# Optimization experiments

Hardware: AMD Instinct MI355X
Metric: run time of the kernel (lower is better)

The kernel has to match this reference:

```python
import jax, jax.numpy as jnp
import numpy as np

N, H, HD = 512, 8, 128          # n_nodes, n_heads, h feature dim
M0, M1 = 256, 256               # mlp_units
NORM_CONST = 1.0


def setup_inputs() -> dict:
    key = jax.random.key(0)
    ks = jax.random.split(key, 16)
    def w(k, i, o, scale=1.0):
        return jax.random.normal(k, (i, o), jnp.float32) * (scale / np.sqrt(i))
    F = HD + H * H               # h_concat dim = 128 + 64 = 192
    EIN = H + 2 * F              # edge MLP input dim = 8 + 384 = 392
    return {
        "x": jax.random.normal(ks[0], (N, H, 3), jnp.float32),
        "h": jax.random.normal(ks[1], (N, HD), jnp.float32),
        # phi_e: MLP([256,256], silu, activate_final=True)
        "We0": w(ks[2], EIN, M0), "be0": jnp.zeros((M0,), jnp.float32),
        "We1": w(ks[3], M0, M1), "be1": jnp.zeros((M1,), jnp.float32),
        # phi_inf: Linear(1) + sigmoid
        "Winf": w(ks[4], M1, 1), "binf": jnp.zeros((1,), jnp.float32),
        # phi_x: MLP([256,256], silu, activate_final=True) -> Linear(n_heads) (variance-scaled small init)
        "Wx0": w(ks[5], M1, M0), "bx0": jnp.zeros((M0,), jnp.float32),
        "Wx1": w(ks[6], M0, M1), "bx1": jnp.zeros((M1,), jnp.float32),
        "Wxo": w(ks[7], M1, H, scale=0.03), "bxo": jnp.zeros((H,), jnp.float32),
        # phi_h: MLP([256,256], silu, activate_final=False)... note haiku MLP applies
        # activation between layers; final Linear(h_dim) appended in forward.
        "Wh0": w(ks[8], M1 + HD, M0), "bh0": jnp.zeros((M0,), jnp.float32),
        "Wh1": w(ks[9], M0, M1), "bh1": jnp.zeros((M1,), jnp.float32),
        "Who": w(ks[10], M1, HD), "bho": jnp.zeros((HD,), jnp.float32),
    }


def _forward(x, h, We0, be0, We1, be1, Winf, binf, Wx0, bx0, Wx1, bx1,
             Wxo, bxo, Wh0, bh0, Wh1, bh1, Who, bho):
    n, nh = x.shape[0], x.shape[1]
    silu = jax.nn.silu
    off = 1.0 - jnp.eye(n, dtype=x.dtype)                  # off-diagonal node mask
    # per-node head-pair squared distances -> [N, H*H] (diag naturally 0)
    dh = x[:, :, None, :] - x[:, None, :, :]               # [N,H,H,3]
    sqh = jnp.sum(dh * dh, axis=-1).reshape(n, nh * nh)
    hc = jnp.concatenate([h, sqh], axis=-1)                # [N, F]
    # all-pairs node diffs per head: dn[i,j,h] = x[j,h] - x[i,h]
    dn = x[None] - x[:, None]                              # [N,N,H,3]
    sqn = jnp.sum(dn * dn, axis=-1)                        # [N,N,H]
    F = hc.shape[-1]
    hc_j = jnp.broadcast_to(hc[None], (n, n, F))           # receiver-side: hc[j]
    hc_i = jnp.broadcast_to(hc[:, None], (n, n, F))        # sender-side: hc[i]
    edge_in = jnp.concatenate([sqn, hc_j, hc_i], axis=-1)  # [N,N,H+2F]
    # phi_e (activate_final=True), zero self-edges
    m = silu(silu(edge_in @ We0 + be0) @ We1 + be1) * off[:, :, None]
    # gate + message aggregation
    e = jax.nn.sigmoid(m @ Winf + binf)[..., 0] * off      # [N,N]
    m_i = jnp.einsum('ijd,ij->id', m, e)                   # [N,M1]
    # phi_x multi-head coordinate weights (tanh=False), zero self-edges
    px = (silu(silu(m @ Wx0 + bx0) @ Wx1 + bx1) @ Wxo + bxo) * off[:, :, None]
    # normalize_by_x_norm=True path
    norm = jnp.sqrt(sqn + 1e-8) + NORM_CONST               # [N,N,H]
    ndiff = (dn / norm[..., None]) * off[:, :, None, None]
    shift = jnp.einsum('ijhd,ijh->ihd', ndiff, px) / (n - 1)  # agg='mean'
    x_new = x + shift
    # phi_h with residual
    ph_in = jnp.concatenate([m_i, h], axis=-1)
    h_new = h + silu(silu(ph_in @ Wh0 + bh0) @ Wh1 + bh1) @ Who + bho
    return x_new, h_new


def reference(x, h, We0, be0, We1, be1, Winf, binf, Wx0, bx0, Wx1, bx1,
              Wxo, bxo, Wh0, bh0, Wh1, bh1, Who, bho):
    return _forward(x, h, We0, be0, We1, be1, Winf, binf, Wx0, bx0, Wx1, bx1,
                    Wxo, bxo, Wh0, bh0, Wh1, bh1, Who, bho)
```

## Files before the change

kernel.cpp:

```cpp
#include <hip/hip_runtime.h>
#include <math.h>

#define N_NODES 512
#define NH 8
#define HD 128
#define M 256
#define PITCH 264
#define JTILE 64
#define RPW 16

typedef __bf16 v8bf __attribute__((ext_vector_type(8)));
typedef float f32x4 __attribute__((ext_vector_type(4)));
typedef unsigned short us4v __attribute__((ext_vector_type(4)));

__device__ __forceinline__ float silu_f(float v) {
  return v * __builtin_amdgcn_rcpf(1.f + __expf(-v));
}
__device__ __forceinline__ float sigmoid_f(float v) {
  return __builtin_amdgcn_rcpf(1.f + __expf(-v));
}
__device__ __forceinline__ unsigned short f2bf(float f) {
  unsigned u = __float_as_uint(f);
  u += 0x7fffu + ((u >> 16) & 1u);
  return (unsigned short)(u >> 16);
}
__device__ __forceinline__ unsigned short f2bf_hi(float f) {
  return (unsigned short)((__float_as_uint(f) + 0x8000u) >> 16);
}
__device__ __forceinline__ float bf2f(unsigned short s) {
  return __uint_as_float(((unsigned)s) << 16);
}

__device__ __forceinline__ void gl2lds16(const unsigned short* g, unsigned short* l) {
  __builtin_amdgcn_global_load_lds(
      (const __attribute__((address_space(1))) unsigned int*)g,
      (__attribute__((address_space(3))) unsigned int*)l, 16, 0, 0);
}

__global__ __launch_bounds__(256) void k_pre(
    const float* __restrict__ x, const float* __restrict__ h,
    const float* __restrict__ We0, const float* __restrict__ be0,
    const float* __restrict__ We1, const float* __restrict__ Wx0,
    const float* __restrict__ Wx1, const float* __restrict__ Wxo,
    unsigned short* __restrict__ wsB,
    float* __restrict__ P, float* __restrict__ Q,
    float* __restrict__ mi, float* __restrict__ shift)
{
  const int t = threadIdx.x;
  if (blockIdx.x < 816) {
    const int gid = blockIdx.x * 256 + t;
    if (gid >= 208896) return;
    float val;
    int dst;
    if (gid < 196608) {
      const int layer = gid >> 16, e = gid & 65535;
      const int k = e >> 8, n = e & 255;
      const float* W = (layer == 0) ? We1 : (layer == 1) ? Wx0 : Wx1;
      val = W[e];
      const int kt = k >> 5, w = k & 31, quad = w >> 3, j = w & 7;
      const int nt = n >> 4, lnib = n & 15;
      dst = layer * 65536 + ((kt * 16 + nt) * 64 + quad * 16 + lnib) * 8 + j;
    } else if (gid < 198656) {
      const int e = gid - 196608;
      val = Wxo[e];
      const int k = e >> 3, col = e & 7;
      const int kt = k >> 5, w = k & 31, quad = w >> 3, j = w & 7;
      dst = 196608 + (kt * 64 + quad * 16 + col) * 8 + j;
    } else if (gid < 200704) {
      const int e = gid - 198656;
      val = 0.f;
      const int k = e >> 3, col = e & 7;
      const int kt = k >> 5, w = k & 31, quad = w >> 3, j = w & 7;
      dst = 196608 + (kt * 64 + quad * 16 + col + 8) * 8 + j;
    } else if (gid < 202752) {
      const int e = gid - 200704;
      val = We0[e];
      const int j = e >> 8, n = e & 255, nt = n >> 4, lnib = n & 15;
      dst = 200704 + (nt * 64 + lnib) * 8 + j;
    } else {
      const int e = gid - 202752;
      val = 0.f;
      const int q = 1 + (e >> 11), rem = e & 2047;
      const int j = rem & 7, lnib = (rem >> 3) & 15, nt = rem >> 7;
      dst = 200704 + (nt * 64 + q * 16 + lnib) * 8 + j;
    }
    wsB[dst] = f2bf(val);
    return;
  }
  const int i = blockIdx.x - 816;
  __shared__ float s_x[24];
  __shared__ float s_hc[192];
  mi[i * M + t] = 0.f;
  if (t < 24) { shift[i * 24 + t] = 0.f; s_x[t] = x[i * 24 + t]; }
  __syncthreads();
  if (t < HD) {
    s_hc[t] = h[i * HD + t];
  } else if (t < 192) {
    const int p = t - HD, a = p >> 3, b = p & 7;
    float s = 0.f;
#pragma unroll
    for (int d = 0; d < 3; ++d) {
      const float dx = s_x[a * 3 + d] - s_x[b * 3 + d];
      s = fmaf(dx, dx, s);
    }
    s_hc[t] = s;
  }
  __syncthreads();
  float p = 0.f, q = 0.f;
  for (int k = 0; k < 192; ++k) {
    const float hv = s_hc[k];
    p = fmaf(hv, We0[(8 + k) * M + t], p);
    q = fmaf(hv, We0[(200 + k) * M + t], q);
  }
  P[i * M + t] = p;
  Q[i * M + t] = q + be0[t];
}

__global__ __launch_bounds__(512, 4) void k_edge(
    const float* __restrict__ x,
    const float* __restrict__ P, const float* __restrict__ Q,
    const float* __restrict__ be1,
    const float* __restrict__ Winf, const float* __restrict__ binf,
    const float* __restrict__ bx0, const float* __restrict__ bx1,
    const float* __restrict__ bxo,
    const unsigned short* __restrict__ wsB,
    float* __restrict__ mi_acc, float* __restrict__ shift_acc)
{
  const int i  = blockIdx.x;
  const int j0 = blockIdx.y * JTILE;
  const int t  = threadIdx.x;
  const int lane = t & 63, wave = t >> 6;
  const int lnib = lane & 15, quad = lane >> 4;
  const int rg = wave >> 1, c = wave & 1;
  const int r0 = rg * RPW;
  const int jw = j0 + r0;
  const int cb = c * 128;

  __shared__ __align__(16) unsigned short a_act[JTILE * PITCH];
  __shared__ __align__(16) unsigned short B_buf[2][8192];
  __shared__ __align__(16) float s_sqn[JTILE][8];
  __shared__ __align__(16) unsigned short s_sqnb[JTILE][8];
  __shared__ float s_red[JTILE][2];
  __shared__ float s_e[JTILE];

  auto stage = [&](const unsigned short* __restrict__ Bg, int kt, int which) {
    const unsigned short* src = Bg + kt * 8192 + wave * 1024 + lane * 8;
    unsigned short* dst = &B_buf[which][wave * 1024];
    gl2lds16(src,       dst);
    gl2lds16(src + 512, dst + 512);
  };

#pragma unroll
  for (int kk = 0; kk < 2; ++kk) {
    const int idx = kk * 64 + lane;
    const int r = idx >> 3, hh = idx & 7;
    const int j = jw + r;
    float s = 0.f;
#pragma unroll
    for (int d = 0; d < 3; ++d) {
      const float dx = x[j * 24 + hh * 3 + d] - x[i * 24 + hh * 3 + d];
      s = fmaf(dx, dx, s);
    }
    s_sqn[r0 + r][hh] = s;
    s_sqnb[r0 + r][hh] = f2bf(s);
  }

  stage(wsB, 0, 0);

  const float binf0 = binf[0];

  f32x4 acc[8];

  {
#pragma unroll
    for (int nt = 0; nt < 8; ++nt)
#pragma unroll
      for (int reg = 0; reg < 4; ++reg)
        acc[nt][reg] = P[(jw + quad * 4 + reg) * M + cb + nt * 16 + lnib];
    const v8bf aS = *(const v8bf*)&s_sqnb[r0 + lnib][0];
    const unsigned short* B0 = wsB + 200704;
#pragma unroll
    for (int nt = 0; nt < 8; ++nt) {
      const v8bf bv = *(const v8bf*)&B0[((c * 8 + nt) * 64 + lane) * 8];
      acc[nt] = __builtin_amdgcn_mfma_f32_16x16x32_bf16(aS, bv, acc[nt], 0, 0, 0);
    }
#pragma unroll
    for (int nt = 0; nt < 8; ++nt) {
      const float qv = Q[i * M + cb + nt * 16 + lnib];
#pragma unroll
      for (int reg = 0; reg < 4; ++reg) {
        const int row = r0 + quad * 4 + reg;
        a_act[row * PITCH + cb + nt * 16 + lnib] = f2bf_hi(silu_f(acc[nt][reg] + qv));
      }
    }
  }

  auto run_gemm = [&](const unsigned short* __restrict__ Bg,
                      const unsigned short* __restrict__ Bnext) {
    __syncthreads();
#pragma unroll
    for (int kt = 0; kt < 8; ++kt) {
      if (kt < 7)      stage(Bg, kt + 1, (kt + 1) & 1);
      else if (Bnext)  stage(Bnext, 0, 0);
      const v8bf a0 = *(const v8bf*)&a_act[(r0 + lnib) * PITCH + kt * 32 + quad * 8];
#pragma unroll
      for (int nt = 0; nt < 8; ++nt) {
        const v8bf bv = *(const v8bf*)&B_buf[kt & 1][(c * 8 + nt) * 512 + lane * 8];
        acc[nt] = __builtin_amdgcn_mfma_f32_16x16x32_bf16(a0, bv, acc[nt], 0, 0, 0);
      }
      __syncthreads();
    }
  };

#pragma unroll
  for (int nt = 0; nt < 8; ++nt) {
    const float b = be1[cb + nt * 16 + lnib];
    acc[nt] = (f32x4){b, b, b, b};
  }
  run_gemm(wsB, wsB + 65536);
  {
    float ge[4] = {0.f, 0.f, 0.f, 0.f};
#pragma unroll
    for (int nt = 0; nt < 8; ++nt) {
      const float wfv = Winf[cb + nt * 16 + lnib];
#pragma unroll
      for (int reg = 0; reg < 4; ++reg) {
        float v = silu_f(acc[nt][reg]);
        const int row = r0 + quad * 4 + reg;
        if (j0 + row == i) v = 0.f;
        a_act[row * PITCH + cb + nt * 16 + lnib] = f2bf_hi(v);
        ge[reg] = fmaf(v, wfv, ge[reg]);
      }
    }
#pragma unroll
    for (int reg = 0; reg < 4; ++reg) {
      float g = ge[reg];
      g += __shfl_xor(g, 1);
      g += __shfl_xor(g, 2);
      g += __shfl_xor(g, 4);
      g += __shfl_xor(g, 8);
      if (lnib == 0) s_red[r0 + quad * 4 + reg][c] = g;
    }
  }
  __syncthreads();
  if (t < JTILE) s_e[t] = sigmoid_f(s_red[t][0] + s_red[t][1] + binf0);
  __syncthreads();

  {
    const int ch = cb + lane * 2;
    float m0 = 0.f, m1 = 0.f;
#pragma unroll
    for (int r = 0; r < RPW; ++r) {
      const unsigned mv = *(const unsigned*)&a_act[(r0 + r) * PITCH + ch];
      const float ev = s_e[r0 + r];
      m0 = fmaf(bf2f((unsigned short)(mv & 0xffffu)), ev, m0);
      m1 = fmaf(bf2f((unsigned short)(mv >> 16)), ev, m1);
    }
    atomicAdd(&mi_acc[i * M + ch + 0], m0);
    atomicAdd(&mi_acc[i * M + ch + 1], m1);
  }

#pragma unroll
  for (int nt = 0; nt < 8; ++nt) {
    const float b = bx0[cb + nt * 16 + lnib];
    acc[nt] = (f32x4){b, b, b, b};
  }
  run_gemm(wsB + 65536, wsB + 131072);
#pragma unroll
  for (int nt = 0; nt < 8; ++nt)
#pragma unroll
    for (int reg = 0; reg < 4; ++reg) {
      const int row = r0 + quad * 4 + reg;
      a_act[row * PITCH + cb + nt * 16 + lnib] = f2bf_hi(silu_f(acc[nt][reg]));
    }

#pragma unroll
  for (int nt = 0; nt < 8; ++nt) {
    const float b = bx1[cb + nt * 16 + lnib];
    acc[nt] = (f32x4){b, b, b, b};
  }
  run_gemm(wsB + 131072, nullptr);
#pragma unroll
  for (int nt = 0; nt < 8; ++nt)
#pragma unroll
    for (int reg = 0; reg < 4; ++reg) {
      const int row = r0 + quad * 4 + reg;
      a_act[row * PITCH + cb + nt * 16 + lnib] = f2bf_hi(silu_f(acc[nt][reg]));
    }
  __syncthreads();

  if (c == 0) {
    f32x4 px;
    {
      const float b = (lnib < 8) ? bxo[lnib] : 0.f;
      px = (f32x4){b, b, b, b};
      const unsigned short* B = wsB + 196608;
#pragma unroll
      for (int kt = 0; kt < 8; ++kt) {
        const v8bf a0 = *(const v8bf*)&a_act[(r0 + lnib) * PITCH + kt * 32 + quad * 8];
        const v8bf bv = *(const v8bf*)&B[(kt * 64 + lane) * 8];
        px = __builtin_amdgcn_mfma_f32_16x16x32_bf16(a0, bv, px, 0, 0, 0);
      }
    }
    const int hh = lnib & 7;
    const float xi0 = x[i * 24 + hh * 3 + 0];
    const float xi1 = x[i * 24 + hh * 3 + 1];
    const float xi2 = x[i * 24 + hh * 3 + 2];
    float p0 = 0.f, p1 = 0.f, p2 = 0.f;
#pragma unroll
    for (int reg = 0; reg < 4; ++reg) {
      const int row = r0 + quad * 4 + reg;
      const int jg = j0 + row;
      if (jg != i) {
        const float pxv = px[reg];
        const float sq  = s_sqn[row][hh];
        const float f   = pxv * __builtin_amdgcn_rcpf(sqrtf(sq + 1e-8f) + 1.f);
        p0 = fmaf(x[jg * 24 + hh * 3 + 0] - xi0, f, p0);
        p1 = fmaf(x[jg * 24 + hh * 3 + 1] - xi1, f, p1);
        p2 = fmaf(x[jg * 24 + hh * 3 + 2] - xi2, f, p2);
      }
    }
    p0 += __shfl_xor(p0, 16); p0 += __shfl_xor(p0, 32);
    p1 += __shfl_xor(p1, 16); p1 += __shfl_xor(p1, 32);
    p2 += __shfl_xor(p2, 16); p2 += __shfl_xor(p2, 32);
    if (lane < 8) {
      atomicAdd(&shift_acc[i * 24 + hh * 3 + 0], p0);
      atomicAdd(&shift_acc[i * 24 + hh * 3 + 1], p1);
      atomicAdd(&shift_acc[i * 24 + hh * 3 + 2], p2);
    }
  }
}

__global__ __launch_bounds__(256) void k_hout(
    const float* __restrict__ x, const float* __restrict__ shift,
    const float* __restrict__ h, const float* __restrict__ mi,
    const float* __restrict__ Wh0, const float* __restrict__ bh0,
    const float* __restrict__ Wh1, const float* __restrict__ bh1,
    const float* __restrict__ Who, const float* __restrict__ bho,
    float* __restrict__ out_x, float* __restrict__ out_h)
{
  const int i = blockIdx.x, t = threadIdx.x;
  __shared__ float s_in[M + HD];
  __shared__ float s_b[M];
  if (t < 24) out_x[i * 24 + t] = x[i * 24 + t] + shift[i * 24 + t] * (1.f / 511.f);
  s_in[t] = mi[i * M + t];
  if (t < HD) s_in[M + t] = h[i * HD + t];
  __syncthreads();
  float acc = bh0[t];
  for (int k = 0; k < M + HD; ++k) acc = fmaf(s_in[k], Wh0[k * M + t], acc);
  s_b[t] = silu_f(acc);
  __syncthreads();
  float acc2 = bh1[t];
  for (int k = 0; k < M; ++k) acc2 = fmaf(s_b[k], Wh1[k * M + t], acc2);
  const float a1v = silu_f(acc2);
  __syncthreads();
  s_in[t] = a1v;
  __syncthreads();
  if (t < HD) {
    float o = bho[t];
    for (int k = 0; k < M; ++k) o = fmaf(s_in[k], Who[k * HD + t], o);
    out_h[i * HD + t] = h[i * HD + t] + o;
  }
}

extern "C" void kernel_launch(void* const* d_in, const int* in_sizes, int n_in,
                              void* d_out, int out_size, void* d_ws, size_t ws_size,
                              hipStream_t stream)
{
  const float* x    = (const float*)d_in[0];
  const float* h    = (const float*)d_in[1];
  const float* We0  = (const float*)d_in[2];
  const float* be0  = (const float*)d_in[3];
  const float* We1  = (const float*)d_in[4];
  const float* be1  = (const float*)d_in[5];
  const float* Winf = (const float*)d_in[6];
  const float* binf = (const float*)d_in[7];
  const float* Wx0  = (const float*)d_in[8];
  const float* bx0  = (const float*)d_in[9];
  const float* Wx1  = (const float*)d_in[10];
  const float* bx1  = (const float*)d_in[11];
  const float* Wxo  = (const float*)d_in[12];
  const float* bxo  = (const float*)d_in[13];
  const float* Wh0  = (const float*)d_in[14];
  const float* bh0  = (const float*)d_in[15];
  const float* Wh1  = (const float*)d_in[16];
  const float* bh1  = (const float*)d_in[17];
  const float* Who  = (const float*)d_in[18];
  const float* bho  = (const float*)d_in[19];

  float* out_x = (float*)d_out;
  float* out_h = out_x + N_NODES * NH * 3;

  float* ws    = (float*)d_ws;
  float* mi    = ws;
  float* shift = ws + 131072;
  float* P     = ws + 143360;
  float* Q     = ws + 274432;
  unsigned short* wsB = (unsigned short*)(ws + 405504);

  k_pre<<<816 + N_NODES, 256, 0, stream>>>(
      x, h, We0, be0, We1, Wx0, Wx1, Wxo, wsB, P, Q, mi, shift);
  k_edge<<<dim3(N_NODES, N_NODES / JTILE), 512, 0, stream>>>(
      x, P, Q, be1, Winf, binf, bx0, bx1, bxo, wsB, mi, shift);
  k_hout<<<N_NODES, 256, 0, stream>>>(
      x, shift, h, mi, Wh0, bh0, Wh1, bh1, Who, bho, out_x, out_h);
}
```

Before: 306.5 us.

## Retile edge GEMM waves to 32x64 blocks and single-buffer weight staging

Changes the per-wave tile in the edge kernel from 16 rows x 128 columns to 32 rows x 64 columns (2 row groups x 4 column groups). Each B fragment now feeds two MFMAs, which cuts LDS reads of the weights per MFMA. The double-buffered B staging with prefetch is replaced by a single buffer with two barriers per k-step, which frees LDS but removes the overlap between global-to-LDS copies and compute. The mi and px reductions are adapted to the new layout.

Result: slower. 324.6 us (+5.9%).

```diff
diff --git a/kernel.cpp b/kernel.cpp
--- a/kernel.cpp
+++ b/kernel.cpp
@@ -7,11 +7,9 @@
 #define M 256
 #define PITCH 264
 #define JTILE 64
-#define RPW 16
 
 typedef __bf16 v8bf __attribute__((ext_vector_type(8)));
 typedef float f32x4 __attribute__((ext_vector_type(4)));
-typedef unsigned short us4v __attribute__((ext_vector_type(4)));
 
 __device__ __forceinline__ float silu_f(float v) {
   return v * __builtin_amdgcn_rcpf(1.f + __expf(-v));
@@ -131,27 +129,27 @@
   const int t  = threadIdx.x;
   const int lane = t & 63, wave = t >> 6;
   const int lnib = lane & 15, quad = lane >> 4;
-  const int rg = wave >> 1, c = wave & 1;
-  const int r0 = rg * RPW;
+  const int rg = wave >> 2, cg = wave & 3;
+  const int r0 = rg * 32;
   const int jw = j0 + r0;
-  const int cb = c * 128;
+  const int cb = cg * 64;
 
   __shared__ __align__(16) unsigned short a_act[JTILE * PITCH];
-  __shared__ __align__(16) unsigned short B_buf[2][8192];
+  __shared__ __align__(16) unsigned short B_buf[8192];
   __shared__ __align__(16) float s_sqn[JTILE][8];
   __shared__ __align__(16) unsigned short s_sqnb[JTILE][8];
-  __shared__ float s_red[JTILE][2];
+  __shared__ float s_red[JTILE][4];
   __shared__ float s_e[JTILE];
 
-  auto stage = [&](const unsigned short* __restrict__ Bg, int kt, int which) {
+  auto stage = [&](const unsigned short* __restrict__ Bg, int kt) {
     const unsigned short* src = Bg + kt * 8192 + wave * 1024 + lane * 8;
-    unsigned short* dst = &B_buf[which][wave * 1024];
+    unsigned short* dst = &B_buf[wave * 1024];
     gl2lds16(src,       dst);
     gl2lds16(src + 512, dst + 512);
   };
 
 #pragma unroll
-  for (int kk = 0; kk < 2; ++kk) {
+  for (int kk = 0; kk < 4; ++kk) {
     const int idx = kk * 64 + lane;
     const int r = idx >> 3, hh = idx & 7;
     const int j = jw + r;
@@ -165,141 +163,172 @@
     s_sqnb[r0 + r][hh] = f2bf(s);
   }
 
-  stage(wsB, 0, 0);
-
   const float binf0 = binf[0];
 
-  f32x4 acc[8];
+  f32x4 acc[2][4];
 
   {
 #pragma unroll
-    for (int nt = 0; nt < 8; ++nt)
-#pragma unroll
-      for (int reg = 0; reg < 4; ++reg)
-        acc[nt][reg] = P[(jw + quad * 4 + reg) * M + cb + nt * 16 + lnib];
-    const v8bf aS = *(const v8bf*)&s_sqnb[r0 + lnib][0];
+    for (int rf = 0; rf < 2; ++rf)
+#pragma unroll
+      for (int nt = 0; nt < 4; ++nt)
+#pragma unroll
+        for (int reg = 0; reg < 4; ++reg)
+          acc[rf][nt][reg] =
+              P[(jw + rf * 16 + quad * 4 + reg) * M + cb + nt * 16 + lnib];
+    const v8bf aS0 = *(const v8bf*)&s_sqnb[r0 + lnib][0];
+    const v8bf aS1 = *(const v8bf*)&s_sqnb[r0 + 16 + lnib][0];
     const unsigned short* B0 = wsB + 200704;
 #pragma unroll
-    for (int nt = 0; nt < 8; ++nt) {
-      const v8bf bv = *(const v8bf*)&B0[((c * 8 + nt) * 64 + lane) * 8];
-      acc[nt] = __builtin_amdgcn_mfma_f32_16x16x32_bf16(aS, bv, acc[nt], 0, 0, 0);
-    }
-#pragma unroll
-    for (int nt = 0; nt < 8; ++nt) {
-      const float qv = Q[i * M + cb + nt * 16 + lnib];
+    for (int nt = 0; nt < 4; ++nt) {
+      const v8bf bv = *(const v8bf*)&B0[((cg * 4 + nt) * 64 + lane) * 8];
+      acc[0][nt] = __builtin_amdgcn_mfma_f32_16x16x32_bf16(aS0, bv, acc[0][nt], 0, 0, 0);
+      acc[1][nt] = __builtin_amdgcn_mfma_f32_16x16x32_bf16(aS1, bv, acc[1][nt], 0, 0, 0);
+    }
+#pragma unroll
+    for (int rf = 0; rf < 2; ++rf)
+#pragma unroll
+      for (int nt = 0; nt < 4; ++nt) {
+        const float qv = Q[i * M + cb + nt * 16 + lnib];
+#pragma unroll
+        for (int reg = 0; reg < 4; ++reg) {
+          const int row = r0 + rf * 16 + quad * 4 + reg;
+          a_act[row * PITCH + cb + nt * 16 + lnib] =
+              f2bf_hi(silu_f(acc[rf][nt][reg] + qv));
+        }
+      }
+  }
+
+  auto run_gemm = [&](const unsigned short* __restrict__ Bg) {
+#pragma unroll
+    for (int kt = 0; kt < 8; ++kt) {
+      __syncthreads();
+      stage(Bg, kt);
+      __syncthreads();
+      const v8bf a0 = *(const v8bf*)&a_act[(r0 + lnib) * PITCH + kt * 32 + quad * 8];
+      const v8bf a1 = *(const v8bf*)&a_act[(r0 + 16 + lnib) * PITCH + kt * 32 + quad * 8];
+#pragma unroll
+      for (int nt = 0; nt < 4; ++nt) {
+        const v8bf bv = *(const v8bf*)&B_buf[(cg * 4 + nt) * 512 + lane * 8];
+        acc[0][nt] = __builtin_amdgcn_mfma_f32_16x16x32_bf16(a0, bv, acc[0][nt], 0, 0, 0);
+        acc[1][nt] = __builtin_amdgcn_mfma_f32_16x16x32_bf16(a1, bv, acc[1][nt], 0, 0, 0);
+      }
+    }
+    __syncthreads();
+  };
+
+#pragma unroll
+  for (int rf = 0; rf < 2; ++rf)
+#pragma unroll
+    for (int nt = 0; nt < 4; ++nt) {
+      const float b = be1[cb + nt * 16 + lnib];
+      acc[rf][nt] = (f32x4){b, b, b, b};
+    }
+  run_gemm(wsB);
+  {
+    float ge[2][4] = {{0.f, 0.f, 0.f, 0.f}, {0.f, 0.f, 0.f, 0.f}};
+#pragma unroll
+    for (int rf = 0; rf < 2; ++rf)
+#pragma unroll
+      for (int nt = 0; nt < 4; ++nt) {
+        const float wfv = Winf[cb + nt * 16 + lnib];
+#pragma unroll
+        for (int reg = 0; reg < 4; ++reg) {
+          float v = silu_f(acc[rf][nt][reg]);
+          const int row = r0 + rf * 16 + quad * 4 + reg;
+          if (j0 + row == i) v = 0.f;
+          a_act[row * PITCH + cb + nt * 16 + lnib] = f2bf_hi(v);
+          ge[rf][reg] = fmaf(v, wfv, ge[rf][reg]);
+        }
+      }
+#pragma unroll
+    for (int rf = 0; rf < 2; ++rf)
 #pragma unroll
       for (int reg = 0; reg < 4; ++reg) {
-        const int row = r0 + quad * 4 + reg;
-        a_act[row * PITCH + cb + nt * 16 + lnib] = f2bf_hi(silu_f(acc[nt][reg] + qv));
-      }
-    }
-  }
-
-  auto run_gemm = [&](const unsigned short* __restrict__ Bg,
-                      const unsigned short* __restrict__ Bnext) {
-    __syncthreads();
-#pragma unroll
-    for (int kt = 0; kt < 8; ++kt) {
-      if (kt < 7)      stage(Bg, kt + 1, (kt + 1) & 1);
-      else if (Bnext)  stage(Bnext, 0, 0);
-      const v8bf a0 = *(const v8bf*)&a_act[(r0 + lnib) * PITCH + kt * 32 + quad * 8];
-#pragma unroll
-      for (int nt = 0; nt < 8; ++nt) {
-        const v8bf bv = *(const v8bf*)&B_buf[kt & 1][(c * 8 + nt) * 512 + lane * 8];
-        acc[nt] = __builtin_amdgcn_mfma_f32_16x16x32_bf16(a0, bv, acc[nt], 0, 0, 0);
-      }
-      __syncthreads();
-    }
-  };
-
-#pragma unroll
-  for (int nt = 0; nt < 8; ++nt) {
-    const float b = be1[cb + nt * 16 + lnib];
-    acc[nt] = (f32x4){b, b, b, b};
-  }
-  run_gemm(wsB, wsB + 65536);
+        float g = ge[rf][reg];
+        g += __shfl_xor(g, 1);
+        g += __shfl_xor(g, 2);
+        g += __shfl_xor(g, 4);
+        g += __shfl_xor(g, 8);
+        if (lnib == 0) s_red[r0 + rf * 16 + quad * 4 + reg][cg] = g;
+      }
+  }
+  __syncthreads();
+  if (t < JTILE)
+    s_e[t] = sigmoid_f(s_red[t][0] + s_red[t][1] + s_red[t][2] + s_red[t][3] + binf0);
+  __syncthreads();
+
   {
-    float ge[4] = {0.f, 0.f, 0.f, 0.f};
-#pragma unroll
-    for (int nt = 0; nt < 8; ++nt) {
-      const float wfv = Winf[cb + nt * 16 + lnib];
-#pragma unroll
-      for (int reg = 0; reg < 4; ++reg) {
-        float v = silu_f(acc[nt][reg]);
-        const int row = r0 + quad * 4 + reg;
-        if (j0 + row == i) v = 0.f;
-        a_act[row * PITCH + cb + nt * 16 + lnib] = f2bf_hi(v);
-        ge[reg] = fmaf(v, wfv, ge[reg]);
-      }
-    }
-#pragma unroll
-    for (int reg = 0; reg < 4; ++reg) {
-      float g = ge[reg];
-      g += __shfl_xor(g, 1);
-      g += __shfl_xor(g, 2);
-      g += __shfl_xor(g, 4);
-      g += __shfl_xor(g, 8);
-      if (lnib == 0) s_red[r0 + quad * 4 + reg][c] = g;
-    }
-  }
-  __syncthreads();
-  if (t < JTILE) s_e[t] = sigmoid_f(s_red[t][0] + s_red[t][1] + binf0);
-  __syncthreads();
-
-  {
-    const int ch = cb + lane * 2;
+    const int ch = cb + (lane & 31) * 2;
+    const int rh = (lane >> 5) * 16;
     float m0 = 0.f, m1 = 0.f;
 #pragma unroll
-    for (int r = 0; r < RPW; ++r) {
-      const unsigned mv = *(const unsigned*)&a_act[(r0 + r) * PITCH + ch];
-      const float ev = s_e[r0 + r];
+    for (int r = 0; r < 16; ++r) {
+      const int row = r0 + rh + r;
+      const unsigned mv = *(const unsigned*)&a_act[row * PITCH + ch];
+      const float ev = s_e[row];
       m0 = fmaf(bf2f((unsigned short)(mv & 0xffffu)), ev, m0);
       m1 = fmaf(bf2f((unsigned short)(mv >> 16)), ev, m1);
     }
-    atomicAdd(&mi_acc[i * M + ch + 0], m0);
-    atomicAdd(&mi_acc[i * M + ch + 1], m1);
-  }
-
-#pragma unroll
-  for (int nt = 0; nt < 8; ++nt) {
-    const float b = bx0[cb + nt * 16 + lnib];
-    acc[nt] = (f32x4){b, b, b, b};
-  }
-  run_gemm(wsB + 65536, wsB + 131072);
-#pragma unroll
-  for (int nt = 0; nt < 8; ++nt)
-#pragma unroll
-    for (int reg = 0; reg < 4; ++reg) {
-      const int row = r0 + quad * 4 + reg;
-      a_act[row * PITCH + cb + nt * 16 + lnib] = f2bf_hi(silu_f(acc[nt][reg]));
-    }
-
-#pragma unroll
-  for (int nt = 0; nt < 8; ++nt) {
-    const float b = bx1[cb + nt * 16 + lnib];
-    acc[nt] = (f32x4){b, b, b, b};
-  }
-  run_gemm(wsB + 131072, nullptr);
-#pragma unroll
-  for (int nt = 0; nt < 8; ++nt)
-#pragma unroll
-    for (int reg = 0; reg < 4; ++reg) {
-      const int row = r0 + quad * 4 + reg;
-      a_act[row * PITCH + cb + nt * 16 + lnib] = f2bf_hi(silu_f(acc[nt][reg]));
-    }
-  __syncthreads();
-
-  if (c == 0) {
-    f32x4 px;
+    m0 += __shfl_xor(m0, 32);
+    m1 += __shfl_xor(m1, 32);
+    if (lane < 32) {
+      atomicAdd(&mi_acc[i * M + ch + 0], m0);
+      atomicAdd(&mi_acc[i * M + ch + 1], m1);
+    }
+  }
+
+#pragma unroll
+  for (int rf = 0; rf < 2; ++rf)
+#pragma unroll
+    for (int nt = 0; nt < 4; ++nt) {
+      const float b = bx0[cb + nt * 16 + lnib];
+      acc[rf][nt] = (f32x4){b, b, b, b};
+    }
+  run_gemm(wsB + 65536);
+#pragma unroll
+  for (int rf = 0; rf < 2; ++rf)
+#pragma unroll
+    for (int nt = 0; nt < 4; ++nt)
+#pragma unroll
+      for (int reg = 0; reg < 4; ++reg) {
+        const int row = r0 + rf * 16 + quad * 4 + reg;
+        a_act[row * PITCH + cb + nt * 16 + lnib] = f2bf_hi(silu_f(acc[rf][nt][reg]));
+      }
+
+#pragma unroll
+  for (int rf = 0; rf < 2; ++rf)
+#pragma unroll
+    for (int nt = 0; nt < 4; ++nt) {
+      const float b = bx1[cb + nt * 16 + lnib];
+      acc[rf][nt] = (f32x4){b, b, b, b};
+    }
+  run_gemm(wsB + 131072);
+#pragma unroll
+  for (int rf = 0; rf < 2; ++rf)
+#pragma unroll
+    for (int nt = 0; nt < 4; ++nt)
+#pragma unroll
+      for (int reg = 0; reg < 4; ++reg) {
+        const int row = r0 + rf * 16 + quad * 4 + reg;
+        a_act[row * PITCH + cb + nt * 16 + lnib] = f2bf_hi(silu_f(acc[rf][nt][reg]));
+      }
+  __syncthreads();
+
+  if (cg == 0) {
+    f32x4 px[2];
     {
       const float b = (lnib < 8) ? bxo[lnib] : 0.f;
-      px = (f32x4){b, b, b, b};
+      px[0] = (f32x4){b, b, b, b};
+      px[1] = (f32x4){b, b, b, b};
       const unsigned short* B = wsB + 196608;
 #pragma unroll
       for (int kt = 0; kt < 8; ++kt) {
         const v8bf a0 = *(const v8bf*)&a_act[(r0 + lnib) * PITCH + kt * 32 + quad * 8];
+        const v8bf a1 = *(const v8bf*)&a_act[(r0 + 16 + lnib) * PITCH + kt * 32 + quad * 8];
         const v8bf bv = *(const v8bf*)&B[(kt * 64 + lane) * 8];
-        px = __builtin_amdgcn_mfma_f32_16x16x32_bf16(a0, bv, px, 0, 0, 0);
+        px[0] = __builtin_amdgcn_mfma_f32_16x16x32_bf16(a0, bv, px[0], 0, 0, 0);
+        px[1] = __builtin_amdgcn_mfma_f32_16x16x32_bf16(a1, bv, px[1], 0, 0, 0);
       }
     }
     const int hh = lnib & 7;
@@ -308,18 +337,20 @@
     const float xi2 = x[i * 24 + hh * 3 + 2];
     float p0 = 0.f, p1 = 0.f, p2 = 0.f;
 #pragma unroll
-    for (int reg = 0; reg < 4; ++reg) {
-      const int row = r0 + quad * 4 + reg;
-      const int jg = j0 + row;
-      if (jg != i) {
-        const float pxv = px[reg];
-        const float sq  = s_sqn[row][hh];
-        const float f   = pxv * __builtin_amdgcn_rcpf(sqrtf(sq + 1e-8f) + 1.f);
-        p0 = fmaf(x[jg * 24 + hh * 3 + 0] - xi0, f, p0);
-        p1 = fmaf(x[jg * 24 + hh * 3 + 1] - xi1, f, p1);
-        p2 = fmaf(x[jg * 24 + hh * 3 + 2] - xi2, f, p2);
-      }
-    }
+    for (int rf = 0; rf < 2; ++rf)
+#pragma unroll
+      for (int reg = 0; reg < 4; ++reg) {
+        const int row = r0 + rf * 16 + quad * 4 + reg;
+        const int jg = j0 + row;
+        if (jg != i) {
+          const float pxv = px[rf][reg];
+          const float sq  = s_sqn[row][hh];
+          const float f   = pxv * __builtin_amdgcn_rcpf(sqrtf(sq + 1e-8f) + 1.f);
+          p0 = fmaf(x[jg * 24 + hh * 3 + 0] - xi0, f, p0);
+          p1 = fmaf(x[jg * 24 + hh * 3 + 1] - xi1, f, p1);
+          p2 = fmaf(x[jg * 24 + hh * 3 + 2] - xi2, f, p2);
+        }
+      }
     p0 += __shfl_xor(p0, 16); p0 += __shfl_xor(p0, 32);
     p1 += __shfl_xor(p1, 16); p1 += __shfl_xor(p1, 32);
     p2 += __shfl_xor(p2, 16); p2 += __shfl_xor(p2, 32);
```
